# Performance work log

Measured on AMD Instinct MI355X. Metric: run time of the kernel, lower is better.

## Reference

```python
import jax, jax.numpy as jnp
import numpy as np

SR = 44100
K = 1.0 / SR                      # time step
LX = 0.5
MAX_OM = 10000.0 * 2.0 * np.pi    # fmax * 2pi
MIN_OM = 20.0 * 2.0 * np.pi
TAU0, TAU1 = 6.0, 1.0
OM2SQ = (2.0 * np.pi * 500.0) ** 2          # OmDamp2^2 (OmDamp1 = 0)
ALPHA = 3.0 * np.log(10.0) / OM2SQ * (OM2SQ / TAU0)   # = 3 ln10 / tau0
BETA = 3.0 * np.log(10.0) / OM2SQ * (1.0 / TAU1 - 1.0 / TAU0)
MU_SCALE, DMU_SCALE, T0MU_SCALE = 2.43, 0.002452, 0.004115
M_MAX = 80  # 80x80 = 6400 modes


def setup_inputs() -> dict:
    z = jnp.zeros((), dtype=jnp.float32)
    return {
        "mu_raw": z, "D_over_mu_raw": z, "T0_over_mu_raw": z,
        "Ly_raw": z, "xo_raw": z, "yo_raw": z,
        "num_samples": 22050,
    }


def _modal_ir(mu_raw, D_over_mu_raw, T0_over_mu_raw, Ly_raw, xo_raw, yo_raw, num_samples):
    sp, sg = jax.nn.softplus, jax.nn.sigmoid
    # physical parameters via differentiable bounds
    mu = (sp(mu_raw) + 1e-4) * MU_SCALE
    D_over_mu = (sp(D_over_mu_raw) + 1e-4) * DMU_SCALE
    T0_over_mu = (sp(T0_over_mu_raw) + 1e-4) * T0MU_SCALE
    Ly = 1.1 + (4.0 - 1.1) * sg(Ly_raw)
    xo = 0.49 * LX + (1.0 - 0.49) * LX * sg(xo_raw)
    yo = 0.51 * Ly + (1.0 - 0.51) * Ly * sg(yo_raw)
    xi = 0.1 * LX
    yi = 0.1 * Ly
    # mode grid [6400]
    idx = jnp.arange(1, M_MAX + 1, dtype=jnp.float32)
    gm, gn = jnp.meshgrid(idx, idx, indexing="ij")
    m, n = gm.ravel(), gn.ravel()
    g1 = (m * np.pi / LX) ** 2 + (n * np.pi / Ly) ** 2
    omega_sq = T0_over_mu * g1 + D_over_mu * g1 * g1
    omega = jnp.sqrt(jax.nn.relu(omega_sq))
    valid = ((omega <= MAX_OM) & (omega >= MIN_OM)).astype(omega.dtype)
    InW = jnp.cos(xi * np.pi * m / LX) * jnp.cos(yi * np.pi * n / Ly)
    OutW = jnp.cos(xo * np.pi * m / LX) * jnp.cos(yo * np.pi * n / Ly)
    sigma = ALPHA + BETA * omega ** 2
    ms = 0.25 * mu * LX * Ly
    P = OutW * InW * (K * K) * jnp.exp(-sigma * K) / ms * valid  # [modes]
    # time axis [T]
    t = jnp.arange(num_samples, dtype=jnp.float32)
    decay_env = jnp.exp(-sigma[:, None] * (t[None, :] - 1.0) * K)    # [modes, T]
    sine_num = jnp.sin(t[None, :] * omega[:, None] * K)              # [modes, T]
    sine_den = jnp.sin(omega * K) + 1e-8                             # [modes]
    mode_waveforms = P[:, None] * decay_env * (sine_num / sine_den[:, None])
    disp = jnp.sum(mode_waveforms, axis=0)                           # [T]
    peak = jnp.max(jnp.abs(disp)) + 1e-8
    return disp / peak


def reference(mu_raw, D_over_mu_raw, T0_over_mu_raw, Ly_raw, xo_raw, yo_raw, num_samples):
    return _modal_ir(mu_raw, D_over_mu_raw, T0_over_mu_raw, Ly_raw, xo_raw, yo_raw, num_samples)
```

## Files before the change

### kernel.cpp

```cpp
#include <hip/hip_runtime.h>
#include <math.h>

#define NMODES 6400
#define TB     128
#define MPT    10
#define NPAIR  5
#define MG     5
#define BATCH  6
#define TC     42

typedef float v2f __attribute__((ext_vector_type(2)));

static __device__ __forceinline__ float softplusf(float x) {
    return log1pf(expf(-fabsf(x))) + fmaxf(x, 0.0f);
}
static __device__ __forceinline__ float sigmoidf(float x) {
    return 1.0f / (1.0f + expf(-x));
}

__global__ void setup_zero_kernel(const float* __restrict__ mu_raw,
                                  const float* __restrict__ Dmu_raw,
                                  const float* __restrict__ T0mu_raw,
                                  const float* __restrict__ Ly_raw,
                                  const float* __restrict__ xo_raw,
                                  const float* __restrict__ yo_raw,
                                  float* __restrict__ wsA,
                                  float* __restrict__ wsW,
                                  float* __restrict__ wsS,
                                  float* __restrict__ wsCW,
                                  float* __restrict__ wsSW,
                                  float* __restrict__ out, int T)
{
    int id = blockIdx.x * blockDim.x + threadIdx.x;
    int gsz = gridDim.x * blockDim.x;
    for (int i = id; i < T; i += gsz) out[i] = 0.0f;
    if (id >= NMODES) return;

    const float KF   = 1.0f / 44100.0f;
    const float PI_F = (float)M_PI;
    const double om2sq = (2.0 * M_PI * 500.0) * (2.0 * M_PI * 500.0);
    const float ALPHA_F  = (float)(3.0 * M_LN10 / om2sq * (om2sq / 6.0));
    const float BETA_F   = (float)(3.0 * M_LN10 / om2sq * (1.0 - 1.0 / 6.0));
    const float MAX_OM_F = (float)(10000.0 * 2.0 * M_PI);
    const float MIN_OM_F = (float)(20.0 * 2.0 * M_PI);
    const float KK_F     = (float)((1.0 / 44100.0) * (1.0 / 44100.0));

    float mu   = (softplusf(mu_raw[0])   + 1e-4f) * 2.43f;
    float Dmu  = (softplusf(Dmu_raw[0])  + 1e-4f) * 0.002452f;
    float T0mu = (softplusf(T0mu_raw[0]) + 1e-4f) * 0.004115f;
    float Ly   = 1.1f + 2.9f * sigmoidf(Ly_raw[0]);
    float xo   = 0.245f + 0.255f * sigmoidf(xo_raw[0]);
    float yo   = __fadd_rn(__fmul_rn(0.51f, Ly),
                           __fmul_rn(__fmul_rn(0.49f, Ly), sigmoidf(yo_raw[0])));

    float mf = (float)(id / 80 + 1);
    float nf = (float)(id % 80 + 1);

    float am = __fmul_rn(__fmul_rn(mf, PI_F), 2.0f);
    float bn = __fdiv_rn(__fmul_rn(nf, PI_F), Ly);
    float g1 = __fadd_rn(__fmul_rn(am, am), __fmul_rn(bn, bn));
    float omega_sq = __fadd_rn(__fmul_rn(T0mu, g1),
                               __fmul_rn(__fmul_rn(Dmu, g1), g1));
    float omega = sqrtf(fmaxf(omega_sq, 0.0f));
    float valid = (omega <= MAX_OM_F && omega >= MIN_OM_F) ? 1.0f : 0.0f;

    float xi_pi = (float)(0.05 * M_PI);
    float yi = __fmul_rn(0.1f, Ly);
    float InW = __fmul_rn(
        cosf(__fmul_rn(__fmul_rn(xi_pi, mf), 2.0f)),
        cosf(__fdiv_rn(__fmul_rn(__fmul_rn(yi, PI_F), nf), Ly)));
    float OutW = __fmul_rn(
        cosf(__fmul_rn(__fmul_rn(__fmul_rn(xo, PI_F), mf), 2.0f)),
        cosf(__fdiv_rn(__fmul_rn(__fmul_rn(yo, PI_F), nf), Ly)));

    float sigma = __fadd_rn(ALPHA_F, __fmul_rn(BETA_F, __fmul_rn(omega, omega)));
    float ms = __fmul_rn(__fmul_rn(__fmul_rn(0.25f, mu), 0.5f), Ly);
    float P = __fmul_rn(
        __fdiv_rn(__fmul_rn(__fmul_rn(__fmul_rn(OutW, InW), KK_F),
                            expf(__fmul_rn(-sigma, KF))),
                  ms),
        valid);
    float den = __fadd_rn(sinf(__fmul_rn(omega, KF)), 1e-8f);
    float A = __fdiv_rn(P, den);

    const double Kd = 1.0 / 44100.0;
    double th = (double)omega * Kd;
    double dd = exp(-(double)sigma * Kd);
    wsA[id]  = A;
    wsW[id]  = omega;
    wsS[id]  = sigma;
    wsCW[id] = (float)(dd * cos(th));
    wsSW[id] = (float)(dd * sin(th));
}

__global__ __launch_bounds__(TB) void accum_kernel(
    const float* __restrict__ wsA,
    const float* __restrict__ wsW,
    const float* __restrict__ wsS,
    const float* __restrict__ wsCW,
    const float* __restrict__ wsSW,
    float* __restrict__ out, int T)
{
    const int tid  = threadIdx.x;
    const int t0   = blockIdx.x * TC;
    const int base = blockIdx.y * (TB * MPT);

    const float  KF     = 1.0f / 44100.0f;
    const double Kd     = 1.0 / 44100.0;
    const double TWO_PI = 6.283185307179586476925286766559;
    const double I2PI   = 0.15915494309189533576888376337251;

    v2f S[NPAIR], C[NPAIR], CW[NPAIR], SW[NPAIR];
    #pragma unroll
    for (int p = 0; p < NPAIR; ++p) {
        int m = base + p * (TB * 2) + tid * 2;
        CW[p] = *(const v2f*)(wsCW + m);
        SW[p] = *(const v2f*)(wsSW + m);
        v2f A  = *(const v2f*)(wsA + m);
        v2f w  = *(const v2f*)(wsW + m);
        v2f sg = *(const v2f*)(wsS + m);
        #pragma unroll
        for (int k = 0; k < 2; ++k) {
            double ph = (double)t0 * (double)w[k] * Kd;
            double q  = rint(ph * I2PI);
            float  r  = (float)fma(-q, TWO_PI, ph);
            float s0, c0;
            __sincosf(r, &s0, &c0);
            float env = A[k] * __expf(-sg[k] * (float)(t0 - 1) * KF);
            S[p][k] = env * s0;
            C[p][k] = env * c0;
        }
    }

    const int lane = tid & 63;

    #pragma unroll 1
    for (int it = 0; it < TC; it += BATCH) {
        float acc[BATCH];
        #pragma unroll
        for (int b = 0; b < BATCH; ++b) {
            v2f s01 = S[0] + S[1];
            v2f s23 = S[2] + S[3];
            v2f sp  = (s01 + s23) + S[4];
            acc[b] = sp[0] + sp[1];
            #pragma unroll
            for (int p = 0; p < NPAIR; ++p) {
                v2f nS = __builtin_elementwise_fma(S[p], CW[p], C[p] * SW[p]);
                v2f nC = __builtin_elementwise_fma(C[p], CW[p], -(S[p] * SW[p]));
                S[p] = nS;
                C[p] = nC;
            }
        }
        #pragma unroll
        for (int off = 32; off > 0; off >>= 1) {
            #pragma unroll
            for (int b = 0; b < BATCH; ++b)
                acc[b] += __shfl_xor(acc[b], off, 64);
        }
        if (lane == 0) {
            int t = t0 + it;
            #pragma unroll
            for (int b = 0; b < BATCH; ++b)
                if (t + b < T) atomicAdd(&out[t + b], acc[b]);
        }
    }
}

__global__ __launch_bounds__(1024) void norm_kernel(float* __restrict__ out, int T)
{
    __shared__ float red[16];
    __shared__ float peakv;
    float mx = 0.0f;
    for (int i = threadIdx.x; i < T; i += 1024) mx = fmaxf(mx, fabsf(out[i]));
    #pragma unroll
    for (int off = 32; off > 0; off >>= 1)
        mx = fmaxf(mx, __shfl_xor(mx, off, 64));
    int lane = threadIdx.x & 63, wv = threadIdx.x >> 6;
    if (lane == 0) red[wv] = mx;
    __syncthreads();
    if (threadIdx.x == 0) {
        float m = red[0];
        #pragma unroll
        for (int i = 1; i < 16; ++i) m = fmaxf(m, red[i]);
        peakv = m + 1e-8f;
    }
    __syncthreads();
    float pk = peakv;
    for (int i = threadIdx.x; i < T; i += 1024) out[i] = __fdiv_rn(out[i], pk);
}

extern "C" void kernel_launch(void* const* d_in, const int* in_sizes, int n_in,
                              void* d_out, int out_size, void* d_ws, size_t ws_size,
                              hipStream_t stream)
{
    const float* mu   = (const float*)d_in[0];
    const float* Dmu  = (const float*)d_in[1];
    const float* T0mu = (const float*)d_in[2];
    const float* Lyr  = (const float*)d_in[3];
    const float* xor_ = (const float*)d_in[4];
    const float* yor_ = (const float*)d_in[5];
    float* out = (float*)d_out;

    float* ws   = (float*)d_ws;
    float* wsA  = ws;
    float* wsW  = ws + NMODES;
    float* wsS  = ws + 2 * NMODES;
    float* wsCW = ws + 3 * NMODES;
    float* wsSW = ws + 4 * NMODES;

    int T = out_size;
    int tchunks = (T + TC - 1) / TC;

    setup_zero_kernel<<<(NMODES + 255) / 256, 256, 0, stream>>>(
        mu, Dmu, T0mu, Lyr, xor_, yor_, wsA, wsW, wsS, wsCW, wsSW, out, T);
    accum_kernel<<<dim3(tchunks, MG), TB, 0, stream>>>(wsA, wsW, wsS, wsCW, wsSW, out, T);
    norm_kernel<<<1, 1024, 0, stream>>>(out, T);
}
```

Baseline: 102.2 us.

## Reduce time-chunk partials via LDS and split normalization into multi-block kernels

The accumulation kernel now writes each thread's per-timestep partial sum into shared memory. After one barrier, 42 threads sum the 128 partials for each timestep, replacing the per-batch 64-lane shuffle reductions and per-wave atomics. The single-block normalization kernel is replaced by a grid-wide max kernel that uses an atomicMax on the float bits (valid because the values are non-negative), followed by a separate grid-wide divide kernel. This trades shuffle and serial single-block work for LDS traffic, one extra kernel launch, and a global atomic.

Measured after the change: 92.41 us. 1.11x faster.

```diff
diff --git a/kernel.cpp b/kernel.cpp
--- a/kernel.cpp
+++ b/kernel.cpp
@@ -29,11 +29,13 @@
                                   float* __restrict__ wsS,
                                   float* __restrict__ wsCW,
                                   float* __restrict__ wsSW,
+                                  unsigned int* __restrict__ peak,
                                   float* __restrict__ out, int T)
 {
     int id = blockIdx.x * blockDim.x + threadIdx.x;
     int gsz = gridDim.x * blockDim.x;
     for (int i = id; i < T; i += gsz) out[i] = 0.0f;
+    if (id == 0) *peak = 0u;
     if (id >= NMODES) return;
 
     const float KF   = 1.0f / 44100.0f;
@@ -101,6 +103,8 @@
     const float* __restrict__ wsSW,
     float* __restrict__ out, int T)
 {
+    __shared__ __align__(16) float lds[TC][TB + 2];
+
     const int tid  = threadIdx.x;
     const int t0   = blockIdx.x * TC;
     const int base = blockIdx.y * (TB * MPT);
@@ -132,17 +136,14 @@
         }
     }
 
-    const int lane = tid & 63;
-
     #pragma unroll 1
     for (int it = 0; it < TC; it += BATCH) {
-        float acc[BATCH];
         #pragma unroll
         for (int b = 0; b < BATCH; ++b) {
             v2f s01 = S[0] + S[1];
             v2f s23 = S[2] + S[3];
             v2f sp  = (s01 + s23) + S[4];
-            acc[b] = sp[0] + sp[1];
+            lds[it + b][tid] = sp[0] + sp[1];
             #pragma unroll
             for (int p = 0; p < NPAIR; ++p) {
                 v2f nS = __builtin_elementwise_fma(S[p], CW[p], C[p] * SW[p]);
@@ -151,42 +152,60 @@
                 C[p] = nC;
             }
         }
+    }
+    __syncthreads();
+
+    const int wv   = tid >> 6;
+    const int lane = tid & 63;
+    if (lane < TC / 2) {
+        int s = wv * (TC / 2) + lane;
+        v2f z = {0.0f, 0.0f};
         #pragma unroll
-        for (int off = 32; off > 0; off >>= 1) {
-            #pragma unroll
-            for (int b = 0; b < BATCH; ++b)
-                acc[b] += __shfl_xor(acc[b], off, 64);
-        }
-        if (lane == 0) {
-            int t = t0 + it;
-            #pragma unroll
-            for (int b = 0; b < BATCH; ++b)
-                if (t + b < T) atomicAdd(&out[t + b], acc[b]);
-        }
-    }
-}
-
-__global__ __launch_bounds__(1024) void norm_kernel(float* __restrict__ out, int T)
-{
-    __shared__ float red[16];
-    __shared__ float peakv;
+        for (int r = 0; r < TB / 2; ++r)
+            z += *(const v2f*)&lds[s][2 * r];
+        int t = t0 + s;
+        if (t < T) atomicAdd(&out[t], z[0] + z[1]);
+    }
+}
+
+__global__ __launch_bounds__(256) void max_kernel(
+    const float* __restrict__ out,
+    unsigned int* __restrict__ peak, int T)
+{
+    __shared__ float red[4];
+    int i = blockIdx.x * 256 + threadIdx.x;
     float mx = 0.0f;
-    for (int i = threadIdx.x; i < T; i += 1024) mx = fmaxf(mx, fabsf(out[i]));
+    if (2 * i + 1 < T) {
+        v2f v = *(const v2f*)(out + 2 * i);
+        mx = fmaxf(fabsf(v[0]), fabsf(v[1]));
+    } else if (2 * i < T) {
+        mx = fabsf(out[2 * i]);
+    }
     #pragma unroll
     for (int off = 32; off > 0; off >>= 1)
         mx = fmaxf(mx, __shfl_xor(mx, off, 64));
-    int lane = threadIdx.x & 63, wv = threadIdx.x >> 6;
-    if (lane == 0) red[wv] = mx;
+    int lane = threadIdx.x & 63, wvx = threadIdx.x >> 6;
+    if (lane == 0) red[wvx] = mx;
     __syncthreads();
     if (threadIdx.x == 0) {
-        float m = red[0];
-        #pragma unroll
-        for (int i = 1; i < 16; ++i) m = fmaxf(m, red[i]);
-        peakv = m + 1e-8f;
-    }
-    __syncthreads();
-    float pk = peakv;
-    for (int i = threadIdx.x; i < T; i += 1024) out[i] = __fdiv_rn(out[i], pk);
+        float m = fmaxf(fmaxf(red[0], red[1]), fmaxf(red[2], red[3]));
+        atomicMax(peak, __float_as_uint(m));
+    }
+}
+
+__global__ __launch_bounds__(256) void div_kernel(
+    float* __restrict__ out, const unsigned int* __restrict__ peak, int T)
+{
+    float pk = __uint_as_float(*peak) + 1e-8f;
+    int i = blockIdx.x * 256 + threadIdx.x;
+    if (2 * i + 1 < T) {
+        v2f v = *(const v2f*)(out + 2 * i);
+        v[0] = __fdiv_rn(v[0], pk);
+        v[1] = __fdiv_rn(v[1], pk);
+        *(v2f*)(out + 2 * i) = v;
+    } else if (2 * i < T) {
+        out[2 * i] = __fdiv_rn(out[2 * i], pk);
+    }
 }
 
 extern "C" void kernel_launch(void* const* d_in, const int* in_sizes, int n_in,
@@ -207,12 +226,16 @@
     float* wsS  = ws + 2 * NMODES;
     float* wsCW = ws + 3 * NMODES;
     float* wsSW = ws + 4 * NMODES;
+    unsigned int* peak = (unsigned int*)(ws + 5 * NMODES);
 
     int T = out_size;
     int tchunks = (T + TC - 1) / TC;
+    int npairs  = (T + 1) / 2;
+    int nblk    = (npairs + 255) / 256;
 
     setup_zero_kernel<<<(NMODES + 255) / 256, 256, 0, stream>>>(
-        mu, Dmu, T0mu, Lyr, xor_, yor_, wsA, wsW, wsS, wsCW, wsSW, out, T);
+        mu, Dmu, T0mu, Lyr, xor_, yor_, wsA, wsW, wsS, wsCW, wsSW, peak, out, T);
     accum_kernel<<<dim3(tchunks, MG), TB, 0, stream>>>(wsA, wsW, wsS, wsCW, wsSW, out, T);
-    norm_kernel<<<1, 1024, 0, stream>>>(out, T);
-}
+    max_kernel<<<nblk, 256, 0, stream>>>(out, peak, T);
+    div_kernel<<<nblk, 256, 0, stream>>>(out, peak, T);
+}
```
